# Kernel tuning notes

Hardware: AMD Instinct MI355X
Metric: run time of the kernel (lower is better)

## Reference

```python
import jax, jax.numpy as jnp
import numpy as np

EPS_LN = 1e-5
EPS_NORM = 1e-12


def _layernorm(h, g, b):
    mu = jnp.mean(h, axis=-1, keepdims=True)
    var = jnp.mean((h - mu) ** 2, axis=-1, keepdims=True)
    return (h - mu) * jax.lax.rsqrt(var + EPS_LN) * g + b


def _l2norm(h):
    n = jnp.linalg.norm(h, axis=-1, keepdims=True)
    return h / jnp.maximum(n, EPS_NORM)


def setup_inputs() -> dict:
    key = jax.random.key(0)
    ks = jax.random.split(key, 6)
    B, S, D = 8, 4096, 1024
    A, C, dc = 16, 8, 64      # n_anchors, n_comp, d_comp
    apc = A // C              # anchors per compartment = 2
    x = jax.random.normal(ks[0], (B, S, D), jnp.float32)
    anchors = jax.random.normal(ks[1], (A, D), jnp.float32)  # normalized inside forward
    ln_g = jnp.ones((D,), jnp.float32)
    ln_b = jnp.zeros((D,), jnp.float32)
    W1 = jax.random.normal(ks[2], (C, apc, 2 * dc), jnp.float32) / np.sqrt(apc)
    b1 = jnp.zeros((C, 2 * dc), jnp.float32)
    W2 = jax.random.normal(ks[3], (C, 2 * dc, dc), jnp.float32) / np.sqrt(2 * dc)
    b2 = jnp.zeros((C, dc), jnp.float32)
    cg = jnp.ones((C, dc), jnp.float32)
    cb = jnp.zeros((C, dc), jnp.float32)
    Wp = jax.random.normal(ks[4], (C * dc, D), jnp.float32) / np.sqrt(C * dc)
    bp = jnp.zeros((D,), jnp.float32)
    gate = jnp.full((D,), -3.0, jnp.float32)  # gate_init = -3.0
    return dict(x=x, anchors=anchors, ln_g=ln_g, ln_b=ln_b, W1=W1, b1=b1,
                W2=W2, b2=b2, cg=cg, cb=cb, Wp=Wp, bp=bp, gate=gate)


def reference(x, anchors, ln_g, ln_b, W1, b1, W2, b2, cg, cb, Wp, bp, gate):
    B, S, D = x.shape
    C, apc, _ = W1.shape
    dc = W2.shape[-1]
    # LayerNorm then L2-normalize each token
    h = _l2norm(_layernorm(x.reshape(B * S, D), ln_g, ln_b))  # (N, D)
    a = _l2norm(anchors)                                      # (A, D)
    tri = 1.0 - h @ a.T                                       # (N, A)
    # asgn = arange(A) % C -> comp k reads columns [k, k+C, ...]
    g = tri.reshape(-1, apc, C)                               # g[:, j, k] = tri[:, j*C + k]
    u = jnp.einsum('nak,kae->nke', g, W1) + b1                # (N, C, 2*dc)
    u = jnp.square(jnp.maximum(u, 0.0))                       # squared ReLU
    y = jnp.einsum('nke,ked->nkd', u, W2) + b2                # (N, C, dc)
    y = _layernorm(y, cg, cb)                                 # per-comp LayerNorm over dc
    y = y.reshape(-1, C * dc)                                 # concat comps in order
    update = (y @ Wp + bp).reshape(B, S, D)
    return x + jax.nn.sigmoid(gate) * update
```

## Files before the change

kernel.cpp:

```cpp
#include <hip/hip_runtime.h>
#include <hip/hip_bf16.h>

#define DIM 1024
#define NANCH 16
#define NCOMP 8
#define DC 64
#define DC2 128
#define EPS_LN 1e-5f
#define EPS_NORM 1e-12f

typedef __bf16 bf16x8 __attribute__((ext_vector_type(8)));
typedef float f32x4 __attribute__((ext_vector_type(4)));

__global__ __launch_bounds__(256) void knorm_anchors(
    const float* __restrict__ anchors, float* __restrict__ An) {
  int a = blockIdx.x, t = threadIdx.x;
  int lane = t & 63, wid = t >> 6;
  __shared__ float red[4];
  float v[4]; float ss = 0.f;
#pragma unroll
  for (int i = 0; i < 4; i++) {
    v[i] = anchors[a * DIM + t + 256 * i];
    ss += v[i] * v[i];
  }
  for (int off = 32; off; off >>= 1) ss += __shfl_down(ss, off);
  if (lane == 0) red[wid] = ss;
  __syncthreads();
  float inv = 1.f / fmaxf(sqrtf(red[0] + red[1] + red[2] + red[3]), EPS_NORM);
#pragma unroll
  for (int i = 0; i < 4; i++) An[a * DIM + t + 256 * i] = v[i] * inv;
}

__global__ __launch_bounds__(256) void ktrans(
    const float* __restrict__ Wp, __hip_bfloat16* __restrict__ WpT) {
  __shared__ float tile[64][65];
  int bj = blockIdx.x, bk = blockIdx.y;
  int tx = threadIdx.x & 63, ty = threadIdx.x >> 6;
#pragma unroll
  for (int i = 0; i < 16; i++) {
    int r = ty + 4 * i;
    tile[r][tx] = Wp[(size_t)(bk * 64 + r) * DIM + bj * 64 + tx];
  }
  __syncthreads();
#pragma unroll
  for (int i = 0; i < 16; i++) {
    int r = ty + 4 * i;
    WpT[(size_t)(bj * 64 + r) * 512 + bk * 64 + tx] = __float2bfloat16(tile[tx][r]);
  }
}

__global__ __launch_bounds__(256) void kprep(
    const float* __restrict__ W2, const float* __restrict__ An,
    __hip_bfloat16* __restrict__ W2B, __hip_bfloat16* __restrict__ AnB) {
  int id = blockIdx.x * 256 + threadIdx.x;
  if (id < 65536) {
    int j = id & 7, lane = (id >> 3) & 63, ks = (id >> 9) & 3,
        nt = (id >> 11) & 3, k = id >> 13;
    int e = ks * 32 + (lane >> 4) * 8 + j;
    int n = nt * 16 + (lane & 15);
    W2B[id] = __float2bfloat16(W2[k * (DC2 * DC) + e * DC + n]);
  } else {
    int id2 = id - 65536;
    int j = id2 & 7, lane = (id2 >> 3) & 63, ks = id2 >> 9;
    int e = ks * 32 + (lane >> 4) * 8 + j;
    int a = lane & 15;
    AnB[id2] = __float2bfloat16(An[a * DIM + e]);
  }
}

#define LDA_H 1032
__global__ __launch_bounds__(256) void ktoken(
    const float* __restrict__ x, const __hip_bfloat16* __restrict__ AnB,
    const float* __restrict__ ln_g, const float* __restrict__ ln_b,
    const float* __restrict__ W1, const float* __restrict__ b1,
    const __hip_bfloat16* __restrict__ W2B, const float* __restrict__ b2,
    const float* __restrict__ cg, const float* __restrict__ cb,
    __hip_bfloat16* __restrict__ yout) {
  int t = threadIdx.x;
  int lane = t & 63, w = t >> 6;
  int l15 = lane & 15, quad = lane >> 4;
  int n0 = blockIdx.x * 16;

  __shared__ __hip_bfloat16 hu[16 * LDA_H];
  __shared__ float tri_s[16 * 16];
  __shared__ float part[4 * 64 * 4];

  float gv[16], bv[16];
#pragma unroll
  for (int i = 0; i < 16; i++) { gv[i] = ln_g[i * 64 + lane]; bv[i] = ln_b[i * 64 + lane]; }
#pragma unroll
  for (int it = 0; it < 4; it++) {
    int tok = w * 4 + it;
    const float* xr = x + (size_t)(n0 + tok) * DIM;
    float xv[16], s = 0.f, s2 = 0.f;
#pragma unroll
    for (int i = 0; i < 16; i++) {
      float v = xr[i * 64 + lane];
      xv[i] = v; s += v; s2 += v * v;
    }
#pragma unroll
    for (int off = 32; off; off >>= 1) { s += __shfl_xor(s, off); s2 += __shfl_xor(s2, off); }
    float mu = s * (1.f / DIM);
    float rstd = rsqrtf(s2 * (1.f / DIM) - mu * mu + EPS_LN);
    float ss = 0.f;
#pragma unroll
    for (int i = 0; i < 16; i++) {
      float h = (xv[i] - mu) * rstd * gv[i] + bv[i];
      xv[i] = h; ss += h * h;
    }
#pragma unroll
    for (int off = 32; off; off >>= 1) ss += __shfl_xor(ss, off);
    float inv = 1.f / fmaxf(sqrtf(ss), EPS_NORM);
#pragma unroll
    for (int i = 0; i < 16; i++)
      hu[tok * LDA_H + i * 64 + lane] = __float2bfloat16(xv[i] * inv);
  }
  __syncthreads();

  {
    f32x4 tacc = {0.f, 0.f, 0.f, 0.f};
#pragma unroll
    for (int ks = w * 8; ks < w * 8 + 8; ks++) {
      bf16x8 afr = *(const bf16x8*)(&hu[l15 * LDA_H + ks * 32 + quad * 8]);
      bf16x8 bfr = *(const bf16x8*)(&AnB[ks * 512 + lane * 8]);
      tacc = __builtin_amdgcn_mfma_f32_16x16x32_bf16(afr, bfr, tacc, 0, 0, 0);
    }
    *(f32x4*)(&part[(w * 64 + lane) * 4]) = tacc;
  }
  __syncthreads();
  {
    int ln = t & 63, rg = t >> 6;
    float v = part[(0 * 64 + ln) * 4 + rg] + part[(1 * 64 + ln) * 4 + rg] +
              part[(2 * 64 + ln) * 4 + rg] + part[(3 * 64 + ln) * 4 + rg];
    int m = (ln >> 4) * 4 + rg, a = ln & 15;
    tri_s[m * 16 + a] = 1.f - v;
  }
  __syncthreads();

  {
    float w1a[4], w1b[4], b1v[4];
#pragma unroll
    for (int i = 0; i < 4; i++) {
      int idx = i * 256 + t, k = idx >> 7, e = idx & 127;
      w1a[i] = W1[k * 256 + e];
      w1b[i] = W1[k * 256 + 128 + e];
      b1v[i] = b1[idx];
    }
#pragma unroll
    for (int tok = 0; tok < 16; tok++) {
#pragma unroll
      for (int i = 0; i < 4; i++) {
        int idx = i * 256 + t, k = idx >> 7;
        float uu = tri_s[tok * 16 + k] * w1a[i] +
                   tri_s[tok * 16 + 8 + k] * w1b[i] + b1v[i];
        uu = fmaxf(uu, 0.f);
        hu[tok * LDA_H + idx] = __float2bfloat16(uu * uu);
      }
    }
  }
  __syncthreads();

#pragma unroll
  for (int kc = 0; kc < 2; kc++) {
    int k = w * 2 + kc;
    bf16x8 afr[4];
#pragma unroll
    for (int ks = 0; ks < 4; ks++)
      afr[ks] = *(const bf16x8*)(&hu[l15 * LDA_H + k * 128 + ks * 32 + quad * 8]);
    f32x4 acc[4] = {{0,0,0,0},{0,0,0,0},{0,0,0,0},{0,0,0,0}};
#pragma unroll
    for (int nt = 0; nt < 4; nt++) {
#pragma unroll
      for (int ks = 0; ks < 4; ks++) {
        bf16x8 bfr = *(const bf16x8*)(&W2B[(size_t)(((k * 4 + nt) * 4 + ks)) * 512 + lane * 8]);
        acc[nt] = __builtin_amdgcn_mfma_f32_16x16x32_bf16(afr[ks], bfr, acc[nt], 0, 0, 0);
      }
    }
    float vals[4][4], s1[4] = {0,0,0,0}, s2[4] = {0,0,0,0};
#pragma unroll
    for (int nt = 0; nt < 4; nt++) {
      float b2v = b2[k * 64 + nt * 16 + l15];
#pragma unroll
      for (int r = 0; r < 4; r++) {
        float v = acc[nt][r] + b2v;
        vals[nt][r] = v; s1[r] += v; s2[r] += v * v;
      }
    }
#pragma unroll
    for (int r = 0; r < 4; r++) {
#pragma unroll
      for (int off = 1; off < 16; off <<= 1) {
        s1[r] += __shfl_xor(s1[r], off);
        s2[r] += __shfl_xor(s2[r], off);
      }
    }
#pragma unroll
    for (int r = 0; r < 4; r++) {
      float mu = s1[r] * (1.f / DC);
      float rs = rsqrtf(s2[r] * (1.f / DC) - mu * mu + EPS_LN);
      int tokrow = quad * 4 + r;
#pragma unroll
      for (int nt = 0; nt < 4; nt++) {
        int d = nt * 16 + l15;
        float yn = (vals[nt][r] - mu) * rs * cg[k * 64 + d] + cb[k * 64 + d];
        yout[(size_t)(n0 + tokrow) * 512 + k * 64 + d] = __float2bfloat16(yn);
      }
    }
  }
}

#define LDP 72
__global__ __launch_bounds__(256) void kgemm(
    const __hip_bfloat16* __restrict__ Y, const __hip_bfloat16* __restrict__ WpT,
    const float* __restrict__ x, const float* __restrict__ bp,
    const float* __restrict__ gate, float* __restrict__ out) {
  __shared__ alignas(16) __hip_bfloat16 As[128 * LDP];
  __shared__ alignas(16) __hip_bfloat16 Bs[128 * LDP];
  int t = threadIdx.x, lane = t & 63, wid = t >> 6;
  int bm = blockIdx.x, bj = blockIdx.y;
  int wm = (wid >> 1) * 64, wj = (wid & 1) * 64;
  int l15 = lane & 15, quad = lane >> 4;

  f32x4 acc[4][4] = {};

  for (int k0 = 0; k0 < 512; k0 += 64) {
#pragma unroll
    for (int it = 0; it < 4; it++) {
      int c = it * 256 + t;
      int row = c >> 3, col = (c & 7) * 8;
      *(uint4*)(&As[row * LDP + col]) =
          *(const uint4*)(&Y[(size_t)(bm * 128 + row) * 512 + k0 + col]);
      *(uint4*)(&Bs[row * LDP + col]) =
          *(const uint4*)(&WpT[(size_t)(bj * 128 + row) * 512 + k0 + col]);
    }
    __syncthreads();
#pragma unroll
    for (int kk = 0; kk < 64; kk += 32) {
      bf16x8 af[4], bfr[4];
#pragma unroll
      for (int i = 0; i < 4; i++) {
        af[i]  = *(const bf16x8*)(&As[(wm + i * 16 + l15) * LDP + kk + quad * 8]);
        bfr[i] = *(const bf16x8*)(&Bs[(wj + i * 16 + l15) * LDP + kk + quad * 8]);
      }
#pragma unroll
      for (int i = 0; i < 4; i++)
#pragma unroll
        for (int j = 0; j < 4; j++)
          acc[i][j] = __builtin_amdgcn_mfma_f32_16x16x32_bf16(af[i], bfr[j], acc[i][j], 0, 0, 0);
    }
    __syncthreads();
  }

  float sg[4], bpv[4];
#pragma unroll
  for (int j = 0; j < 4; j++) {
    int gc = bj * 128 + wj + j * 16 + l15;
    sg[j] = 1.f / (1.f + expf(-gate[gc]));
    bpv[j] = bp[gc];
  }
#pragma unroll
  for (int i = 0; i < 4; i++) {
#pragma unroll
    for (int j = 0; j < 4; j++) {
      int gc = bj * 128 + wj + j * 16 + l15;
#pragma unroll
      for (int r = 0; r < 4; r++) {
        int gr = bm * 128 + wm + i * 16 + quad * 4 + r;
        size_t idx = (size_t)gr * DIM + gc;
        out[idx] = x[idx] + sg[j] * (acc[i][j][r] + bpv[j]);
      }
    }
  }
}

extern "C" void kernel_launch(void* const* d_in, const int* in_sizes, int n_in,
                              void* d_out, int out_size, void* d_ws, size_t ws_size,
                              hipStream_t stream) {
  const float* x       = (const float*)d_in[0];
  const float* anchors = (const float*)d_in[1];
  const float* ln_g    = (const float*)d_in[2];
  const float* ln_b    = (const float*)d_in[3];
  const float* W1      = (const float*)d_in[4];
  const float* b1      = (const float*)d_in[5];
  const float* W2      = (const float*)d_in[6];
  const float* b2      = (const float*)d_in[7];
  const float* cg      = (const float*)d_in[8];
  const float* cb      = (const float*)d_in[9];
  const float* Wp      = (const float*)d_in[10];
  const float* bp      = (const float*)d_in[11];
  const float* gate    = (const float*)d_in[12];

  int N = in_sizes[0] / DIM;

  char* w = (char*)d_ws;
  size_t off = 0;
  float* An           = (float*)(w + off);           off += 64 << 10;
  __hip_bfloat16* WpT = (__hip_bfloat16*)(w + off);  off += 1 << 20;
  __hip_bfloat16* W2B = (__hip_bfloat16*)(w + off);  off += 128 << 10;
  __hip_bfloat16* AnB = (__hip_bfloat16*)(w + off);  off += 32 << 10;
  __hip_bfloat16* Yb  = (__hip_bfloat16*)(w + off);

  knorm_anchors<<<NANCH, 256, 0, stream>>>(anchors, An);
  ktrans<<<dim3(16, 8), 256, 0, stream>>>(Wp, WpT);
  kprep<<<320, 256, 0, stream>>>(W2, An, W2B, AnB);
  ktoken<<<N / 16, 256, 0, stream>>>(x, AnB, ln_g, ln_b, W1, b1, W2B, b2, cg, cb, Yb);
  kgemm<<<dim3(N / 128, DIM / 128), 256, 0, stream>>>(Yb, WpT, x, bp, gate,
                                                      (float*)d_out);
}
```

Measured before the change: 357.7 us.

## Halve tokens per ktoken block and vectorize x/LN-param loads

The token kernel now processes 8 tokens per block instead of 16, halving LDS use, doubling the grid, and adding a launch-bounds occupancy hint of 7 blocks per CU. The MFMA tiles still use 16 rows; rows 8-15 alias rows 0-7 and their results are discarded. Loads of x and the LayerNorm parameters become float4-vectorized, and the bf16 LDS stores are packed four at a time. The goal is higher occupancy and memory throughput in this bandwidth-bound kernel, at the cost of wasted MFMA work and more redundant per-block weight loads.

After: 360.3 us. About the same (+0.7%).

```diff
diff --git a/kernel.cpp b/kernel.cpp
--- a/kernel.cpp
+++ b/kernel.cpp
@@ -69,7 +69,7 @@
 }
 
 #define LDA_H 1032
-__global__ __launch_bounds__(256) void ktoken(
+__global__ __launch_bounds__(256, 7) void ktoken(
     const float* __restrict__ x, const __hip_bfloat16* __restrict__ AnB,
     const float* __restrict__ ln_g, const float* __restrict__ ln_b,
     const float* __restrict__ W1, const float* __restrict__ b1,
@@ -79,24 +79,33 @@
   int t = threadIdx.x;
   int lane = t & 63, w = t >> 6;
   int l15 = lane & 15, quad = lane >> 4;
-  int n0 = blockIdx.x * 16;
-
-  __shared__ __hip_bfloat16 hu[16 * LDA_H];
-  __shared__ float tri_s[16 * 16];
+  int n0 = blockIdx.x * 8;
+
+  __shared__ __hip_bfloat16 hu[8 * LDA_H];
+  __shared__ float tri_s[8 * 16];
   __shared__ float part[4 * 64 * 4];
 
   float gv[16], bv[16];
 #pragma unroll
-  for (int i = 0; i < 16; i++) { gv[i] = ln_g[i * 64 + lane]; bv[i] = ln_b[i * 64 + lane]; }
-#pragma unroll
-  for (int it = 0; it < 4; it++) {
-    int tok = w * 4 + it;
+  for (int i = 0; i < 4; i++) {
+    f32x4 g4 = *(const f32x4*)(&ln_g[i * 256 + lane * 4]);
+    f32x4 b4 = *(const f32x4*)(&ln_b[i * 256 + lane * 4]);
+#pragma unroll
+    for (int j = 0; j < 4; j++) { gv[i * 4 + j] = g4[j]; bv[i * 4 + j] = b4[j]; }
+  }
+#pragma unroll
+  for (int it = 0; it < 2; it++) {
+    int tok = w * 2 + it;
     const float* xr = x + (size_t)(n0 + tok) * DIM;
     float xv[16], s = 0.f, s2 = 0.f;
 #pragma unroll
-    for (int i = 0; i < 16; i++) {
-      float v = xr[i * 64 + lane];
-      xv[i] = v; s += v; s2 += v * v;
+    for (int i = 0; i < 4; i++) {
+      f32x4 v4 = *(const f32x4*)(&xr[i * 256 + lane * 4]);
+#pragma unroll
+      for (int j = 0; j < 4; j++) {
+        float v = v4[j];
+        xv[i * 4 + j] = v; s += v; s2 += v * v;
+      }
     }
 #pragma unroll
     for (int off = 32; off; off >>= 1) { s += __shfl_xor(s, off); s2 += __shfl_xor(s2, off); }
@@ -112,16 +121,21 @@
     for (int off = 32; off; off >>= 1) ss += __shfl_xor(ss, off);
     float inv = 1.f / fmaxf(sqrtf(ss), EPS_NORM);
 #pragma unroll
-    for (int i = 0; i < 16; i++)
-      hu[tok * LDA_H + i * 64 + lane] = __float2bfloat16(xv[i] * inv);
+    for (int i = 0; i < 4; i++) {
+      union { uint2 u; __hip_bfloat16 h[4]; } pk;
+#pragma unroll
+      for (int j = 0; j < 4; j++) pk.h[j] = __float2bfloat16(xv[i * 4 + j] * inv);
+      *(uint2*)(&hu[tok * LDA_H + i * 256 + lane * 4]) = pk.u;
+    }
   }
   __syncthreads();
 
   {
     f32x4 tacc = {0.f, 0.f, 0.f, 0.f};
+    int ar = l15 & 7;
 #pragma unroll
     for (int ks = w * 8; ks < w * 8 + 8; ks++) {
-      bf16x8 afr = *(const bf16x8*)(&hu[l15 * LDA_H + ks * 32 + quad * 8]);
+      bf16x8 afr = *(const bf16x8*)(&hu[ar * LDA_H + ks * 32 + quad * 8]);
       bf16x8 bfr = *(const bf16x8*)(&AnB[ks * 512 + lane * 8]);
       tacc = __builtin_amdgcn_mfma_f32_16x16x32_bf16(afr, bfr, tacc, 0, 0, 0);
     }
@@ -133,7 +147,7 @@
     float v = part[(0 * 64 + ln) * 4 + rg] + part[(1 * 64 + ln) * 4 + rg] +
               part[(2 * 64 + ln) * 4 + rg] + part[(3 * 64 + ln) * 4 + rg];
     int m = (ln >> 4) * 4 + rg, a = ln & 15;
-    tri_s[m * 16 + a] = 1.f - v;
+    if (m < 8) tri_s[m * 16 + a] = 1.f - v;
   }
   __syncthreads();
 
@@ -147,7 +161,7 @@
       b1v[i] = b1[idx];
     }
 #pragma unroll
-    for (int tok = 0; tok < 16; tok++) {
+    for (int tok = 0; tok < 8; tok++) {
 #pragma unroll
       for (int i = 0; i < 4; i++) {
         int idx = i * 256 + t, k = idx >> 7;
@@ -163,10 +177,11 @@
 #pragma unroll
   for (int kc = 0; kc < 2; kc++) {
     int k = w * 2 + kc;
+    int ar = l15 & 7;
     bf16x8 afr[4];
 #pragma unroll
     for (int ks = 0; ks < 4; ks++)
-      afr[ks] = *(const bf16x8*)(&hu[l15 * LDA_H + k * 128 + ks * 32 + quad * 8]);
+      afr[ks] = *(const bf16x8*)(&hu[ar * LDA_H + k * 128 + ks * 32 + quad * 8]);
     f32x4 acc[4] = {{0,0,0,0},{0,0,0,0},{0,0,0,0},{0,0,0,0}};
 #pragma unroll
     for (int nt = 0; nt < 4; nt++) {
@@ -199,11 +214,13 @@
       float mu = s1[r] * (1.f / DC);
       float rs = rsqrtf(s2[r] * (1.f / DC) - mu * mu + EPS_LN);
       int tokrow = quad * 4 + r;
-#pragma unroll
-      for (int nt = 0; nt < 4; nt++) {
-        int d = nt * 16 + l15;
-        float yn = (vals[nt][r] - mu) * rs * cg[k * 64 + d] + cb[k * 64 + d];
-        yout[(size_t)(n0 + tokrow) * 512 + k * 64 + d] = __float2bfloat16(yn);
+      if (tokrow < 8) {
+#pragma unroll
+        for (int nt = 0; nt < 4; nt++) {
+          int d = nt * 16 + l15;
+          float yn = (vals[nt][r] - mu) * rs * cg[k * 64 + d] + cb[k * 64 + d];
+          yout[(size_t)(n0 + tokrow) * 512 + k * 64 + d] = __float2bfloat16(yn);
+        }
       }
     }
   }
@@ -303,7 +320,7 @@
   knorm_anchors<<<NANCH, 256, 0, stream>>>(anchors, An);
   ktrans<<<dim3(16, 8), 256, 0, stream>>>(Wp, WpT);
   kprep<<<320, 256, 0, stream>>>(W2, An, W2B, AnB);
-  ktoken<<<N / 16, 256, 0, stream>>>(x, AnB, ln_g, ln_b, W1, b1, W2B, b2, cg, cb, Yb);
+  ktoken<<<N / 8, 256, 0, stream>>>(x, AnB, ln_g, ln_b, W1, b1, W2B, b2, cg, cb, Yb);
   kgemm<<<dim3(N / 128, DIM / 128), 256, 0, stream>>>(Yb, WpT, x, bp, gate,
                                                       (float*)d_out);
 }
```
